# Kernel tuning notes

Hardware: AMD Instinct MI355X
Metric: run time of the kernel (lower is better)

Reference implementation:

```python
import jax, jax.numpy as jnp
import numpy as np

D = 128          # embedding_size
K = 1024         # num_embedding
DECAY = 0.99
EPS = 1e-5
VQ_COMMIT = 0.25
B, T = 16, 4096


def setup_inputs() -> dict:
    key = jax.random.key(0)
    k1, k2, k3 = jax.random.split(key, 3)
    emb = jax.random.normal(k2, (D, K), dtype=jnp.float32)
    return {
        "input": jax.random.normal(k1, (B, T, D), dtype=jnp.float32),
        "embedding": emb,
        "cluster_size": jnp.zeros((K,), dtype=jnp.float32),
        "embedding_mean": emb.copy(),
    }


def reference(input, embedding, cluster_size, embedding_mean):
    # ---- quantize: squared-distance argmin over codebook ----
    flatten = input.reshape(-1, D)                                   # [N, D]
    dist = ((flatten ** 2).sum(1, keepdims=True)
            - 2.0 * flatten @ embedding
            + (embedding ** 2).sum(0, keepdims=True))                # [N, K]
    embedding_ind = jnp.argmin(dist, axis=1)                         # [N]
    code = embedding_ind.reshape(input.shape[:-1])                   # [B, T]

    # ---- dequantize: codebook gather ----
    quantize = jnp.take(embedding.T, code, axis=0)                   # [B, T, D]

    # ---- EMA codebook update (training mode) ----
    N = flatten.shape[0]
    counts = jax.ops.segment_sum(jnp.ones((N,), input.dtype), embedding_ind,
                                 num_segments=K)                     # [K]
    emb_sum = jax.ops.segment_sum(flatten, embedding_ind,
                                  num_segments=K).T                  # [D, K]
    new_cluster_size = cluster_size * DECAY + (1.0 - DECAY) * counts
    new_embedding_mean = embedding_mean * DECAY + (1.0 - DECAY) * emb_sum
    n = new_cluster_size.sum()
    cs = (new_cluster_size + EPS) / (n + K * EPS) * n
    new_embedding = new_embedding_mean / cs[None, :]                 # [D, K]

    # ---- straight-through estimator + commitment loss ----
    quantize_st = input + jax.lax.stop_gradient(quantize - input)
    diff = VQ_COMMIT * jnp.mean(
        (jax.lax.stop_gradient(quantize_st) - input) ** 2)

    return (quantize_st, diff, code,
            new_embedding, new_cluster_size, new_embedding_mean)
```

## Files before the change

### kernel.cpp

```cpp
#include <hip/hip_runtime.h>
#include <hip/hip_fp16.h>
#include <math.h>

#define D_ 128
#define K_ 1024
#define N_ 65536
#define DECAY_ 0.99f
#define OMD_ 0.01f
#define EPS_ 1e-5f
#define VQC_ 0.25f
#define M1_ 0.14f
#define M2_ 0.14f
#define BIAS_ 96.0f
#define CLMIN_ 0.5f
#define CLMAX_ 508.0f
#define WSEG 32

typedef __attribute__((ext_vector_type(8))) _Float16 half8;
typedef __attribute__((ext_vector_type(4))) float f32x4;

#define WOFF_CODE  0
#define WOFF_E2    65536
#define WOFF_CNT   66560
#define WOFF_SSQ   67584
#define WOFF_RCNT  67585
#define WOFF_BASE  67648
#define WOFF_CURS  68736
#define WOFF_ORDER 69760
#define WOFF_ET    136320
#define WOFF_PART  267392
#define WOFF_CSORT 398464
#define WOFF_RLIST 791680
#define WOFF_EF    857216

#define OOFF_Q     0
#define OOFF_DIFF  8388608
#define OOFF_CODE  8388609
#define OOFF_NEMB  8454145
#define OOFF_NCS   8585217
#define OOFF_NMEAN 8586241

__device__ __forceinline__ unsigned umin32(unsigned a, unsigned b) { return a < b ? a : b; }
__device__ __forceinline__ unsigned umax32(unsigned a, unsigned b) { return a > b ? a : b; }

__device__ __forceinline__ void gld16(const unsigned short* g, unsigned short* l) {
    __builtin_amdgcn_global_load_lds(
        (const __attribute__((address_space(1))) unsigned int*)g,
        (__attribute__((address_space(3))) unsigned int*)l, 16, 0, 0);
}

__launch_bounds__(256)
__global__ void k_prep(const float* __restrict__ E, float* __restrict__ Et,
                       unsigned short* __restrict__ Ef, float* __restrict__ e2,
                       int* __restrict__ cnt, float* __restrict__ part1) {
    __shared__ float tile[128 * 17];
    __shared__ float e2s[16];
    int tid = threadIdx.x;
    int b = blockIdx.x;
    int c0 = b * 16;
    if (b == 0) {
        for (int i = tid; i < 1026; i += 256) cnt[i] = 0;
    }
    #pragma unroll
    for (int i = 0; i < 8; ++i) part1[b * 2048 + i * 256 + tid] = 0.f;
    if (tid < 16) e2s[tid] = 0.f;
    #pragma unroll
    for (int i = 0; i < 8; ++i) {
        int idx = i * 256 + tid;
        int d = idx >> 4, cc = idx & 15;
        tile[d * 17 + cc] = E[d * K_ + c0 + cc];
    }
    __syncthreads();
    #pragma unroll
    for (int i = 0; i < 8; ++i) {
        int idx = i * 256 + tid;
        int cc = idx >> 7, d = idx & 127;
        Et[(size_t)(c0 + cc) * D_ + d] = tile[d * 17 + cc];
    }
    int L = tid & 63, s = tid >> 6;
    int cc = L & 15;
    int d0 = s * 32 + ((L >> 4) << 3);
    unsigned short h[8];
    float sq = 0.f;
    #pragma unroll
    for (int j = 0; j < 8; ++j) {
        float e = tile[(d0 + j) * 17 + cc];
        sq = fmaf(e, e, sq);
        h[j] = __half_as_ushort(__float2half(-2.f * e));
    }
    int T = b * 256 + tid;
    #pragma unroll
    for (int j = 0; j < 8; ++j) Ef[T * 8 + j] = h[j];
    atomicAdd(&e2s[cc], sq);
    __syncthreads();
    if (tid < 16) {
        e2[c0 + tid] = e2s[tid];
    }
}

__launch_bounds__(512, 2)
__global__ void k_argmin_mfma(const float* __restrict__ x, const unsigned short* __restrict__ Ef,
                              const float* __restrict__ e2,
                              int* __restrict__ code_i, float* __restrict__ code_f,
                              int* __restrict__ cnt, int* __restrict__ rcnt,
                              int* __restrict__ rlist, const float* __restrict__ Et) {
    __shared__ unsigned short Bs[3][8192];
    __shared__ float e2s[K_];
    int tid = threadIdx.x;
    int w = tid >> 6, L = tid & 63, quad = L >> 4, col = L & 15;
    int mg = w >> 1, ng = w & 1;
    int n0 = blockIdx.x * 128;

    for (int i = tid; i < K_; i += 512) e2s[i] = e2[i];

    half8 ah[2][4];
    #pragma unroll
    for (int mt = 0; mt < 2; ++mt) {
        int tok = n0 + (2 * mg + mt) * 16 + col;
        #pragma unroll
        for (int s = 0; s < 4; ++s) {
            const float* p = x + (size_t)tok * D_ + s * 32 + quad * 8;
            float4 u0 = *(const float4*)(p);
            float4 u1 = *(const float4*)(p + 4);
            ah[mt][s][0] = (_Float16)u0.x; ah[mt][s][1] = (_Float16)u0.y;
            ah[mt][s][2] = (_Float16)u0.z; ah[mt][s][3] = (_Float16)u0.w;
            ah[mt][s][4] = (_Float16)u1.x; ah[mt][s][5] = (_Float16)u1.y;
            ah[mt][s][6] = (_Float16)u1.z; ah[mt][s][7] = (_Float16)u1.w;
        }
    }

    unsigned k1[2][4], k2[2][4], k3[2][4];
    #pragma unroll
    for (int mt = 0; mt < 2; ++mt)
        #pragma unroll
        for (int r = 0; r < 4; ++r) {
            k1[mt][r] = 0xFFFFFFFFu; k2[mt][r] = 0xFFFFFFFFu; k3[mt][r] = 0xFFFFFFFFu;
        }

    __syncthreads();

    #pragma unroll
    for (int i = 0; i < 2; ++i) {
        int o = (w * 2 + i) * 512;
        gld16(Ef + o + L * 8, &Bs[0][o]);
    }
    #pragma unroll
    for (int i = 0; i < 2; ++i) {
        int o = (w * 2 + i) * 512;
        gld16(Ef + 8192 + o + L * 8, &Bs[1][o]);
    }

    #pragma unroll
    for (int q = 0; q < 16; ++q) {
        if (q < 15) asm volatile("s_waitcnt vmcnt(2)" ::: "memory");
        else        asm volatile("s_waitcnt vmcnt(0)" ::: "memory");
        __builtin_amdgcn_s_barrier();
        asm volatile("" ::: "memory");

        const unsigned short* Bp = &Bs[q % 3][0];

        float evb[2];
        #pragma unroll
        for (int nn = 0; nn < 2; ++nn)
            evb[nn] = e2s[q * 64 + (2 * ng + nn) * 16 + col] + BIAS_;
        f32x4 acc[2][2];
        #pragma unroll
        for (int mt = 0; mt < 2; ++mt)
            #pragma unroll
            for (int nn = 0; nn < 2; ++nn)
                #pragma unroll
                for (int r = 0; r < 4; ++r)
                    acc[mt][nn][r] = evb[nn];

        #pragma unroll
        for (int s = 0; s < 4; ++s) {
            half8 bh[2];
            #pragma unroll
            for (int nn = 0; nn < 2; ++nn) {
                int off = (((2 * ng + nn) * 4 + s) * 64 + L) * 8;
                bh[nn] = *(const half8*)(Bp + off);
            }
            #pragma unroll
            for (int nn = 0; nn < 2; ++nn)
                #pragma unroll
                for (int mt = 0; mt < 2; ++mt)
                    acc[mt][nn] = __builtin_amdgcn_mfma_f32_16x16x32_f16(ah[mt][s], bh[nn], acc[mt][nn], 0, 0, 0);
        }

        #pragma unroll
        for (int nn = 0; nn < 2; ++nn) {
            unsigned cb = (unsigned)(q * 64 + (2 * ng + nn) * 16 + col);
            #pragma unroll
            for (int mt = 0; mt < 2; ++mt)
                #pragma unroll
                for (int r = 0; r < 4; ++r) {
                    float dc = fminf(fmaxf(acc[mt][nn][r], CLMIN_), CLMAX_);
                    unsigned key = (__float_as_uint(dc) & 0xFFFFFC00u) | cb;
                    unsigned m1 = umax32(k1[mt][r], key);
                    k1[mt][r]   = umin32(k1[mt][r], key);
                    unsigned m2 = umax32(k2[mt][r], m1);
                    k2[mt][r]   = umin32(k2[mt][r], m1);
                    k3[mt][r]   = umin32(k3[mt][r], m2);
                }
        }

        if (q < 14) {
            const unsigned short* src = Ef + (q + 2) * 8192;
            int sl = (q + 2) % 3;
            #pragma unroll
            for (int i = 0; i < 2; ++i) {
                int o = (w * 2 + i) * 512;
                gld16(src + o + L * 8, &Bs[sl][o]);
            }
        }
    }

    __syncthreads();
    unsigned* mk1 = (unsigned*)&Bs[0][0];
    unsigned* mk2 = mk1 + 256;
    unsigned* mk3 = mk2 + 256;

    #pragma unroll
    for (int mt = 0; mt < 2; ++mt) {
        #pragma unroll
        for (int r = 0; r < 4; ++r) {
            unsigned a = k1[mt][r], b = k2[mt][r], c = k3[mt][r];
            #pragma unroll
            for (int m = 1; m < 16; m <<= 1) {
                unsigned ao = (unsigned)__shfl_xor((int)a, m);
                unsigned bo = (unsigned)__shfl_xor((int)b, m);
                unsigned co = (unsigned)__shfl_xor((int)c, m);
                unsigned t1 = umax32(a, ao);
                a           = umin32(a, ao);
                unsigned s2 = umin32(b, bo);
                unsigned u  = umax32(t1, s2);
                b           = umin32(t1, s2);
                c           = umin32(u, umin32(c, co));
            }
            if (col == 0) {
                int tl = (2 * mg + mt) * 16 + quad * 4 + r;
                mk1[tl * 2 + ng] = a;
                mk2[tl * 2 + ng] = b;
                mk3[tl * 2 + ng] = c;
            }
        }
    }
    __syncthreads();
    if (tid < 128) {
        unsigned a1 = mk1[tid * 2], b1 = mk1[tid * 2 + 1];
        unsigned a2 = mk2[tid * 2], b2 = mk2[tid * 2 + 1];
        unsigned a3 = mk3[tid * 2], b3 = mk3[tid * 2 + 1];
        unsigned t1 = umax32(a1, b1);
        unsigned kk1 = umin32(a1, b1);
        unsigned s2 = umin32(a2, b2);
        unsigned kk2 = umin32(t1, s2);
        unsigned u  = umax32(t1, s2);
        unsigned kk3 = umin32(u, umin32(a3, b3));

        int i1 = (int)(kk1 & 1023u), i2 = (int)(kk2 & 1023u);
        float d1 = __uint_as_float(kk1 & 0xFFFFFC00u);
        float d2 = __uint_as_float(kk2 & 0xFFFFFC00u);
        float d3 = __uint_as_float(kk3 & 0xFFFFFC00u);
        int tok = n0 + tid;

        if (d3 - d1 < M2_) {
            code_i[tok] = i1;
            code_f[tok] = (float)i1;
            atomicAdd(cnt + i1, 1);
            int p = atomicAdd(rcnt, 1);
            rlist[p] = tok;
        } else {
            int win = i1;
            if (d2 - d1 < M1_) {
                const float* xr = x  + (size_t)tok * D_;
                const float* ea = Et + (size_t)i1 * D_;
                const float* eb = Et + (size_t)i2 * D_;
                float s1 = 0.f, sB = 0.f;
                #pragma unroll 4
                for (int dd = 0; dd < D_; dd += 4) {
                    float4 xv = *(const float4*)(xr + dd);
                    float4 av = *(const float4*)(ea + dd);
                    float4 bv = *(const float4*)(eb + dd);
                    s1 = fmaf(xv.x, av.x, s1); s1 = fmaf(xv.y, av.y, s1);
                    s1 = fmaf(xv.z, av.z, s1); s1 = fmaf(xv.w, av.w, s1);
                    sB = fmaf(xv.x, bv.x, sB); sB = fmaf(xv.y, bv.y, sB);
                    sB = fmaf(xv.z, bv.z, sB); sB = fmaf(xv.w, bv.w, sB);
                }
                float ex1 = e2s[i1] - 2.f * s1;
                float ex2 = e2s[i2] - 2.f * sB;
                if (ex2 < ex1 || (ex2 == ex1 && i2 < i1)) win = i2;
            }
            code_i[tok] = win;
            code_f[tok] = (float)win;
            atomicAdd(cnt + win, 1);
        }
    }
}

__launch_bounds__(256)
__global__ void k_fix(const float* __restrict__ x, const float* __restrict__ Et,
                      const float* __restrict__ e2, const int* __restrict__ rcnt,
                      const int* __restrict__ rlist, int* __restrict__ code_i,
                      float* __restrict__ code_f, int* __restrict__ cnt) {
    __shared__ float4 xs[32];
    __shared__ float sd[8];
    __shared__ int   si[8];
    int tid = threadIdx.x;
    int lane = tid & 63, w = tid >> 6;
    int half = lane >> 5;
    int q32  = lane & 31;
    int slot = w * 2 + half;
    int nr = *rcnt;
    for (int it = blockIdx.x; it < nr; it += gridDim.x) {
        __syncthreads();
        int tok = rlist[it];
        if (tid < 32) xs[tid] = ((const float4*)(x + (size_t)tok * D_))[tid];
        __syncthreads();
        float4 xv = xs[q32];
        float bd = INFINITY; int bb = 0;
        for (int c0 = 0; c0 < K_; c0 += 8) {
            int c = c0 + slot;
            float4 e = ((const float4*)(Et + (size_t)c * D_))[q32];
            float dot = xv.x * e.x + xv.y * e.y + xv.z * e.z + xv.w * e.w;
            dot += __shfl_xor(dot, 1);
            dot += __shfl_xor(dot, 2);
            dot += __shfl_xor(dot, 4);
            dot += __shfl_xor(dot, 8);
            dot += __shfl_xor(dot, 16);
            float dist = e2[c] - 2.f * dot;
            if (dist < bd) { bd = dist; bb = c; }
        }
        if (q32 == 0) { sd[slot] = bd; si[slot] = bb; }
        __syncthreads();
        if (tid == 0) {
            float fb = sd[0]; int fi = si[0];
            #pragma unroll
            for (int s = 1; s < 8; ++s) {
                if (sd[s] < fb || (sd[s] == fb && si[s] < fi)) { fb = sd[s]; fi = si[s]; }
            }
            int ob = code_i[tok];
            if (fi != ob) {
                code_i[tok] = fi;
                code_f[tok] = (float)fi;
                atomicAdd(cnt + ob, -1);
                atomicAdd(cnt + fi, 1);
            }
        }
    }
}

__launch_bounds__(256)
__global__ void k_scan(const int* __restrict__ cnt, int* __restrict__ base,
                       int* __restrict__ cursor) {
    int t = threadIdx.x;
    int lane = t & 63, wv = t >> 6;
    int c[4];
    #pragma unroll
    for (int j = 0; j < 4; ++j) c[j] = cnt[4 * t + j];
    int s = c[0] + c[1] + c[2] + c[3];
    int ps = s;
    #pragma unroll
    for (int m = 1; m < 64; m <<= 1) {
        int o = __shfl_up(ps, m);
        if (lane >= m) ps += o;
    }
    __shared__ int wtot[4];
    if (lane == 63) wtot[wv] = ps;
    __syncthreads();
    int woff = 0;
    for (int i = 0; i < 4; ++i) if (i < wv) woff += wtot[i];
    int run = woff + ps - s;
    #pragma unroll
    for (int j = 0; j < 4; ++j) {
        cursor[4 * t + j] = run;
        run += c[j];
        base[4 * t + j + 1] = run;
    }
    if (t == 0) base[0] = 0;
}

__global__ void k_scatter(const int* __restrict__ code_i, int* __restrict__ cursor,
                          int* __restrict__ order, int* __restrict__ csort) {
    int n = blockIdx.x * 256 + threadIdx.x;
    int c = code_i[n];
    int pos = atomicAdd(cursor + c, 1);
    order[pos] = n;
    csort[pos] = c;
}

__launch_bounds__(128)
__global__ void k_segdeq(const float* __restrict__ x, const float* __restrict__ Et,
                         const int* __restrict__ order, const int* __restrict__ csort,
                         float* __restrict__ part1, float* __restrict__ outq,
                         float* __restrict__ ssqp) {
    __shared__ int sn[WSEG], sc[WSEG];
    int d = threadIdx.x;
    int i0 = blockIdx.x * WSEG;
    if (d < WSEG) { sn[d] = order[i0 + d]; sc[d] = csort[i0 + d]; }
    __syncthreads();
    int cprev = sc[0];
    float eq = Et[(size_t)cprev * D_ + d];
    float acc = 0.f, ssql = 0.f;
    float xv = x[(size_t)sn[0] * D_ + d];
    #pragma unroll 4
    for (int j = 0; j < WSEG; ++j) {
        float xn = (j < WSEG - 1) ? x[(size_t)sn[j + 1] * D_ + d] : 0.f;
        int c = sc[j];
        if (c != cprev) {
            atomicAdd(&part1[(size_t)cprev * D_ + d], acc);
            acc = 0.f;
            eq = Et[(size_t)c * D_ + d];
            cprev = c;
        }
        float qv = xv + (eq - xv);
        outq[(size_t)sn[j] * D_ + d] = qv;
        float t = qv - xv;
        ssql = fmaf(t, t, ssql);
        acc += xv;
        xv = xn;
    }
    atomicAdd(&part1[(size_t)cprev * D_ + d], acc);

    #pragma unroll
    for (int off = 32; off > 0; off >>= 1) ssql += __shfl_down(ssql, off);
    __shared__ float wsum[2];
    if ((d & 63) == 0) wsum[d >> 6] = ssql;
    __syncthreads();
    if (d == 0) atomicAdd(ssqp, wsum[0] + wsum[1]);
}

__launch_bounds__(256)
__global__ void k_embed(const float* __restrict__ em, const float* __restrict__ part1,
                        const int* __restrict__ cnt, const float* __restrict__ csz,
                        const float* __restrict__ ssqp, float* __restrict__ out_nmean,
                        float* __restrict__ out_nemb, float* __restrict__ out_ncs,
                        float* __restrict__ out_diff) {
    int tid = threadIdx.x;
    __shared__ float red[256];

    float ls = 0.f;
    for (int j = tid; j < K_; j += 256) ls += csz[j] * DECAY_ + OMD_ * (float)cnt[j];
    red[tid] = ls;
    __syncthreads();
    for (int off = 128; off > 0; off >>= 1) {
        if (tid < off) red[tid] += red[tid + off];
        __syncthreads();
    }
    float n = red[0];
    __syncthreads();

    if (blockIdx.x == 0) {
        for (int j = tid; j < K_; j += 256)
            out_ncs[j] = csz[j] * DECAY_ + OMD_ * (float)cnt[j];
        if (tid == 0) *out_diff = VQC_ * ssqp[0] / (float)(N_ * D_);
    }

    int i = blockIdx.x * 256 + tid;
    int k = i & (K_ - 1);
    int d = i >> 10;
    float ncs_k = csz[k] * DECAY_ + OMD_ * (float)cnt[k];
    float csk = (ncs_k + EPS_) / (n + (float)K_ * EPS_) * n;
    float es = part1[(size_t)k * D_ + d];
    float nm = em[i] * DECAY_ + OMD_ * es;
    out_nmean[i] = nm;
    out_nemb[i]  = nm / csk;
}

extern "C" void kernel_launch(void* const* d_in, const int* in_sizes, int n_in,
                              void* d_out, int out_size, void* d_ws, size_t ws_size,
                              hipStream_t stream) {
    const float* x   = (const float*)d_in[0];
    const float* E   = (const float*)d_in[1];
    const float* csz = (const float*)d_in[2];
    const float* em  = (const float*)d_in[3];
    float* out = (float*)d_out;
    float* W   = (float*)d_ws;

    int*   code_i = (int*)(W + WOFF_CODE);
    float* e2     = W + WOFF_E2;
    int*   cnt    = (int*)(W + WOFF_CNT);
    float* ssqp   = W + WOFF_SSQ;
    int*   rcnt   = (int*)(W + WOFF_RCNT);
    int*   base   = (int*)(W + WOFF_BASE);
    int*   cursor = (int*)(W + WOFF_CURS);
    int*   order  = (int*)(W + WOFF_ORDER);
    float* Et     = W + WOFF_ET;
    float* part1  = W + WOFF_PART;
    int*   csort  = (int*)(W + WOFF_CSORT);
    int*   rlist  = (int*)(W + WOFF_RLIST);
    unsigned short* Ef = (unsigned short*)(W + WOFF_EF);

    k_prep<<<64, 256, 0, stream>>>(E, Et, Ef, e2, cnt, part1);
    k_argmin_mfma<<<N_ / 128, 512, 0, stream>>>(x, Ef, e2, code_i,
                                                out + OOFF_CODE, cnt, rcnt, rlist, Et);
    k_fix<<<1024, 256, 0, stream>>>(x, Et, e2, rcnt, rlist, code_i, out + OOFF_CODE, cnt);
    k_scan<<<1, 256, 0, stream>>>(cnt, base, cursor);
    k_scatter<<<N_ / 256, 256, 0, stream>>>(code_i, cursor, order, csort);
    k_segdeq<<<N_ / WSEG, 128, 0, stream>>>(x, Et, order, csort, part1,
                                            out + OOFF_Q, ssqp);
    k_embed<<<(D_ * K_) / 256, 256, 0, stream>>>(em, part1, cnt, csz, ssqp,
                                                 out + OOFF_NMEAN, out + OOFF_NEMB,
                                                 out + OOFF_NCS, out + OOFF_DIFF);
}
```

Before: 238.8 us.

## Fuse scan, scatter, segment dequant and EMA update into one cooperative kernel

Replaces four kernel launches (scan, scatter, segmented dequantize/sum, EMA update) with one cooperative kernel of 2048 blocks that uses grid.sync between phases. Each block recomputes the prefix scan into shared memory, so the single-block scan kernel goes away. A separate zeroed counter array replaces the cursor array. Separately, the argmin kernel's launch bound is raised to ask for 4 blocks per CU. This trades launch gaps for grid-wide barriers and needs all 2048 blocks co-resident, and the tighter occupancy target may force register spills in the MFMA argmin.

```diff
diff --git a/kernel.cpp b/kernel.cpp
--- a/kernel.cpp
+++ b/kernel.cpp
@@ -1,6 +1,9 @@
 #include <hip/hip_runtime.h>
 #include <hip/hip_fp16.h>
+#include <hip/hip_cooperative_groups.h>
 #include <math.h>
+
+namespace cg = cooperative_groups;
 
 #define D_ 128
 #define K_ 1024
@@ -15,6 +18,7 @@
 #define CLMIN_ 0.5f
 #define CLMAX_ 508.0f
 #define WSEG 32
+#define CBLK 2048
 
 typedef __attribute__((ext_vector_type(8))) _Float16 half8;
 typedef __attribute__((ext_vector_type(4))) float f32x4;
@@ -52,7 +56,8 @@
 __launch_bounds__(256)
 __global__ void k_prep(const float* __restrict__ E, float* __restrict__ Et,
                        unsigned short* __restrict__ Ef, float* __restrict__ e2,
-                       int* __restrict__ cnt, float* __restrict__ part1) {
+                       int* __restrict__ cnt, int* __restrict__ zc,
+                       float* __restrict__ part1) {
     __shared__ float tile[128 * 17];
     __shared__ float e2s[16];
     int tid = threadIdx.x;
@@ -61,6 +66,9 @@
     if (b == 0) {
         for (int i = tid; i < 1026; i += 256) cnt[i] = 0;
     }
+    if (b == 1) {
+        for (int i = tid; i < 1024; i += 256) zc[i] = 0;
+    }
     #pragma unroll
     for (int i = 0; i < 8; ++i) part1[b * 2048 + i * 256 + tid] = 0.f;
     if (tid < 16) e2s[tid] = 0.f;
@@ -98,7 +106,7 @@
     }
 }
 
-__launch_bounds__(512, 2)
+__launch_bounds__(512, 4)
 __global__ void k_argmin_mfma(const float* __restrict__ x, const unsigned short* __restrict__ Ef,
                               const float* __restrict__ e2,
                               int* __restrict__ code_i, float* __restrict__ code_f,
@@ -349,121 +357,123 @@
     }
 }
 
-__launch_bounds__(256)
-__global__ void k_scan(const int* __restrict__ cnt, int* __restrict__ base,
-                       int* __restrict__ cursor) {
-    int t = threadIdx.x;
-    int lane = t & 63, wv = t >> 6;
-    int c[4];
-    #pragma unroll
-    for (int j = 0; j < 4; ++j) c[j] = cnt[4 * t + j];
-    int s = c[0] + c[1] + c[2] + c[3];
+__launch_bounds__(128)
+__global__ void k_coop(const int* __restrict__ cnt, int* __restrict__ zc,
+                       const int* __restrict__ code_i, int* __restrict__ order,
+                       int* __restrict__ csort, const float* __restrict__ x,
+                       const float* __restrict__ Et, float* __restrict__ part1,
+                       float* __restrict__ outq, float* __restrict__ ssqp,
+                       const float* __restrict__ em, const float* __restrict__ csz,
+                       float* __restrict__ out_nmean, float* __restrict__ out_nemb,
+                       float* __restrict__ out_ncs, float* __restrict__ out_diff) {
+    cg::grid_group grid = cg::this_grid();
+    __shared__ int baseS[1025];
+    __shared__ int sn[WSEG], sc[WSEG];
+    __shared__ float red[128];
+    int tid = threadIdx.x;
+    int bid = blockIdx.x;
+    int lane = tid & 63, wv = tid >> 6;
+
+    int c8[8];
+    #pragma unroll
+    for (int j = 0; j < 8; ++j) c8[j] = cnt[8 * tid + j];
+    int s = 0;
+    #pragma unroll
+    for (int j = 0; j < 8; ++j) s += c8[j];
     int ps = s;
     #pragma unroll
     for (int m = 1; m < 64; m <<= 1) {
         int o = __shfl_up(ps, m);
         if (lane >= m) ps += o;
     }
-    __shared__ int wtot[4];
+    __shared__ int wtot[2];
     if (lane == 63) wtot[wv] = ps;
     __syncthreads();
-    int woff = 0;
-    for (int i = 0; i < 4; ++i) if (i < wv) woff += wtot[i];
+    int woff = (wv == 1) ? wtot[0] : 0;
     int run = woff + ps - s;
     #pragma unroll
-    for (int j = 0; j < 4; ++j) {
-        cursor[4 * t + j] = run;
-        run += c[j];
-        base[4 * t + j + 1] = run;
-    }
-    if (t == 0) base[0] = 0;
-}
-
-__global__ void k_scatter(const int* __restrict__ code_i, int* __restrict__ cursor,
-                          int* __restrict__ order, int* __restrict__ csort) {
-    int n = blockIdx.x * 256 + threadIdx.x;
-    int c = code_i[n];
-    int pos = atomicAdd(cursor + c, 1);
-    order[pos] = n;
-    csort[pos] = c;
-}
-
-__launch_bounds__(128)
-__global__ void k_segdeq(const float* __restrict__ x, const float* __restrict__ Et,
-                         const int* __restrict__ order, const int* __restrict__ csort,
-                         float* __restrict__ part1, float* __restrict__ outq,
-                         float* __restrict__ ssqp) {
-    __shared__ int sn[WSEG], sc[WSEG];
-    int d = threadIdx.x;
-    int i0 = blockIdx.x * WSEG;
-    if (d < WSEG) { sn[d] = order[i0 + d]; sc[d] = csort[i0 + d]; }
-    __syncthreads();
-    int cprev = sc[0];
-    float eq = Et[(size_t)cprev * D_ + d];
-    float acc = 0.f, ssql = 0.f;
-    float xv = x[(size_t)sn[0] * D_ + d];
-    #pragma unroll 4
-    for (int j = 0; j < WSEG; ++j) {
-        float xn = (j < WSEG - 1) ? x[(size_t)sn[j + 1] * D_ + d] : 0.f;
-        int c = sc[j];
-        if (c != cprev) {
-            atomicAdd(&part1[(size_t)cprev * D_ + d], acc);
-            acc = 0.f;
-            eq = Et[(size_t)c * D_ + d];
-            cprev = c;
-        }
-        float qv = xv + (eq - xv);
-        outq[(size_t)sn[j] * D_ + d] = qv;
-        float t = qv - xv;
-        ssql = fmaf(t, t, ssql);
-        acc += xv;
-        xv = xn;
-    }
-    atomicAdd(&part1[(size_t)cprev * D_ + d], acc);
-
-    #pragma unroll
-    for (int off = 32; off > 0; off >>= 1) ssql += __shfl_down(ssql, off);
-    __shared__ float wsum[2];
-    if ((d & 63) == 0) wsum[d >> 6] = ssql;
-    __syncthreads();
-    if (d == 0) atomicAdd(ssqp, wsum[0] + wsum[1]);
-}
-
-__launch_bounds__(256)
-__global__ void k_embed(const float* __restrict__ em, const float* __restrict__ part1,
-                        const int* __restrict__ cnt, const float* __restrict__ csz,
-                        const float* __restrict__ ssqp, float* __restrict__ out_nmean,
-                        float* __restrict__ out_nemb, float* __restrict__ out_ncs,
-                        float* __restrict__ out_diff) {
-    int tid = threadIdx.x;
-    __shared__ float red[256];
-
-    float ls = 0.f;
-    for (int j = tid; j < K_; j += 256) ls += csz[j] * DECAY_ + OMD_ * (float)cnt[j];
-    red[tid] = ls;
-    __syncthreads();
-    for (int off = 128; off > 0; off >>= 1) {
-        if (tid < off) red[tid] += red[tid + off];
+    for (int j = 0; j < 8; ++j) {
+        run += c8[j];
+        baseS[8 * tid + j + 1] = run;
+    }
+    if (tid == 0) baseS[0] = 0;
+    __syncthreads();
+
+    if (bid < 512) {
+        int n = bid * 128 + tid;
+        int c = code_i[n];
+        int pos = baseS[c] + atomicAdd(zc + c, 1);
+        order[pos] = n;
+        csort[pos] = c;
+    }
+    grid.sync();
+
+    {
+        int d = tid;
+        int i0 = bid * WSEG;
+        if (d < WSEG) { sn[d] = order[i0 + d]; sc[d] = csort[i0 + d]; }
         __syncthreads();
-    }
-    float n = red[0];
-    __syncthreads();
-
-    if (blockIdx.x == 0) {
-        for (int j = tid; j < K_; j += 256)
-            out_ncs[j] = csz[j] * DECAY_ + OMD_ * (float)cnt[j];
-        if (tid == 0) *out_diff = VQC_ * ssqp[0] / (float)(N_ * D_);
-    }
-
-    int i = blockIdx.x * 256 + tid;
-    int k = i & (K_ - 1);
-    int d = i >> 10;
-    float ncs_k = csz[k] * DECAY_ + OMD_ * (float)cnt[k];
-    float csk = (ncs_k + EPS_) / (n + (float)K_ * EPS_) * n;
-    float es = part1[(size_t)k * D_ + d];
-    float nm = em[i] * DECAY_ + OMD_ * es;
-    out_nmean[i] = nm;
-    out_nemb[i]  = nm / csk;
+        int cprev = sc[0];
+        float eq = Et[(size_t)cprev * D_ + d];
+        float acc = 0.f, ssql = 0.f;
+        float xv = x[(size_t)sn[0] * D_ + d];
+        #pragma unroll 4
+        for (int j = 0; j < WSEG; ++j) {
+            float xn = (j < WSEG - 1) ? x[(size_t)sn[j + 1] * D_ + d] : 0.f;
+            int c = sc[j];
+            if (c != cprev) {
+                atomicAdd(&part1[(size_t)cprev * D_ + d], acc);
+                acc = 0.f;
+                eq = Et[(size_t)c * D_ + d];
+                cprev = c;
+            }
+            float qv = xv + (eq - xv);
+            outq[(size_t)sn[j] * D_ + d] = qv;
+            float t = qv - xv;
+            ssql = fmaf(t, t, ssql);
+            acc += xv;
+            xv = xn;
+        }
+        atomicAdd(&part1[(size_t)cprev * D_ + d], acc);
+
+        #pragma unroll
+        for (int off = 32; off > 0; off >>= 1) ssql += __shfl_down(ssql, off);
+        __shared__ float wsum[2];
+        if ((d & 63) == 0) wsum[d >> 6] = ssql;
+        __syncthreads();
+        if (d == 0) atomicAdd(ssqp, wsum[0] + wsum[1]);
+    }
+    grid.sync();
+
+    {
+        float ls = 0.f;
+        for (int j = tid; j < K_; j += 128) ls += csz[j] * DECAY_ + OMD_ * (float)cnt[j];
+        red[tid] = ls;
+        __syncthreads();
+        for (int off = 64; off > 0; off >>= 1) {
+            if (tid < off) red[tid] += red[tid + off];
+            __syncthreads();
+        }
+        float n = red[0];
+
+        if (bid == 0) {
+            for (int j = tid; j < K_; j += 128)
+                out_ncs[j] = csz[j] * DECAY_ + OMD_ * (float)cnt[j];
+            if (tid == 0) *out_diff = VQC_ * ssqp[0] / (float)(N_ * D_);
+        }
+
+        if (bid < 1024) {
+            int i = bid * 128 + tid;
+            int k = i & (K_ - 1);
+            int d = i >> 10;
+            float ncs_k = csz[k] * DECAY_ + OMD_ * (float)cnt[k];
+            float csk = (ncs_k + EPS_) / (n + (float)K_ * EPS_) * n;
+            float es = part1[(size_t)k * D_ + d];
+            float nm = em[i] * DECAY_ + OMD_ * es;
+            out_nmean[i] = nm;
+            out_nemb[i]  = nm / csk;
+        }
+    }
 }
 
 extern "C" void kernel_launch(void* const* d_in, const int* in_sizes, int n_in,
@@ -481,8 +491,7 @@
     int*   cnt    = (int*)(W + WOFF_CNT);
     float* ssqp   = W + WOFF_SSQ;
     int*   rcnt   = (int*)(W + WOFF_RCNT);
-    int*   base   = (int*)(W + WOFF_BASE);
-    int*   cursor = (int*)(W + WOFF_CURS);
+    int*   zc     = (int*)(W + WOFF_CURS);
     int*   order  = (int*)(W + WOFF_ORDER);
     float* Et     = W + WOFF_ET;
     float* part1  = W + WOFF_PART;
@@ -490,15 +499,19 @@
     int*   rlist  = (int*)(W + WOFF_RLIST);
     unsigned short* Ef = (unsigned short*)(W + WOFF_EF);
 
-    k_prep<<<64, 256, 0, stream>>>(E, Et, Ef, e2, cnt, part1);
-    k_argmin_mfma<<<N_ / 128, 512, 0, stream>>>(x, Ef, e2, code_i,
-                                                out + OOFF_CODE, cnt, rcnt, rlist, Et);
-    k_fix<<<1024, 256, 0, stream>>>(x, Et, e2, rcnt, rlist, code_i, out + OOFF_CODE, cnt);
-    k_scan<<<1, 256, 0, stream>>>(cnt, base, cursor);
-    k_scatter<<<N_ / 256, 256, 0, stream>>>(code_i, cursor, order, csort);
-    k_segdeq<<<N_ / WSEG, 128, 0, stream>>>(x, Et, order, csort, part1,
-                                            out + OOFF_Q, ssqp);
-    k_embed<<<(D_ * K_) / 256, 256, 0, stream>>>(em, part1, cnt, csz, ssqp,
-                                                 out + OOFF_NMEAN, out + OOFF_NEMB,
-                                                 out + OOFF_NCS, out + OOFF_DIFF);
+    float* code_o = out + OOFF_CODE;
+    float* outq   = out + OOFF_Q;
+    float* nmean  = out + OOFF_NMEAN;
+    float* nemb   = out + OOFF_NEMB;
+    float* ncs    = out + OOFF_NCS;
+    float* diffp  = out + OOFF_DIFF;
+
+    k_prep<<<64, 256, 0, stream>>>(E, Et, Ef, e2, cnt, zc, part1);
+    k_argmin_mfma<<<N_ / 128, 512, 0, stream>>>(x, Ef, e2, code_i, code_o,
+                                                cnt, rcnt, rlist, Et);
+    k_fix<<<1024, 256, 0, stream>>>(x, Et, e2, rcnt, rlist, code_i, code_o, cnt);
+
+    void* args[] = { &cnt, &zc, &code_i, &order, &csort, &x, &Et, &part1,
+                     &outq, &ssqp, &em, &csz, &nmean, &nemb, &ncs, &diffp };
+    hipLaunchCooperativeKernel((void*)k_coop, dim3(CBLK), dim3(128), args, 0, stream);
 }
```

Measured after the change: 556.6 us. 133% more time.

## Load codebook fragments directly from global memory, drop LDS pipeline in argmin

Applied to the files above, without the earlier changes.

The argmin kernel no longer stages codebook tiles into a triple-buffered LDS ring with async global-to-LDS loads and barriers. Each wave now reads its B fragments straight from global memory (L2/L1 cached) and covers all 64 codes per step for its own 32 tokens. The cross-wave top-3 merge goes away because each token is owned by one wave. The block shrinks from 512 to 256 threads. This removes LDS traffic and per-step barriers, but every wave now fetches the whole codebook itself, so global/L2 load traffic rises and load latency is exposed, with only 2x unrolling to hide it.

```diff
diff --git a/kernel.cpp b/kernel.cpp
--- a/kernel.cpp
+++ b/kernel.cpp
@@ -43,12 +43,6 @@
 __device__ __forceinline__ unsigned umin32(unsigned a, unsigned b) { return a < b ? a : b; }
 __device__ __forceinline__ unsigned umax32(unsigned a, unsigned b) { return a > b ? a : b; }
 
-__device__ __forceinline__ void gld16(const unsigned short* g, unsigned short* l) {
-    __builtin_amdgcn_global_load_lds(
-        (const __attribute__((address_space(1))) unsigned int*)g,
-        (__attribute__((address_space(3))) unsigned int*)l, 16, 0, 0);
-}
-
 __launch_bounds__(256)
 __global__ void k_prep(const float* __restrict__ E, float* __restrict__ Et,
                        unsigned short* __restrict__ Ef, float* __restrict__ e2,
@@ -98,25 +92,24 @@
     }
 }
 
-__launch_bounds__(512, 2)
+__launch_bounds__(256)
 __global__ void k_argmin_mfma(const float* __restrict__ x, const unsigned short* __restrict__ Ef,
                               const float* __restrict__ e2,
                               int* __restrict__ code_i, float* __restrict__ code_f,
                               int* __restrict__ cnt, int* __restrict__ rcnt,
                               int* __restrict__ rlist, const float* __restrict__ Et) {
-    __shared__ unsigned short Bs[3][8192];
     __shared__ float e2s[K_];
+    __shared__ unsigned mk1[128], mk2[128], mk3[128];
     int tid = threadIdx.x;
     int w = tid >> 6, L = tid & 63, quad = L >> 4, col = L & 15;
-    int mg = w >> 1, ng = w & 1;
-    int n0 = blockIdx.x * 128;
-
-    for (int i = tid; i < K_; i += 512) e2s[i] = e2[i];
+    int n0 = blockIdx.x * 128 + w * 32;
+
+    for (int i = tid; i < K_; i += 256) e2s[i] = e2[i];
 
     half8 ah[2][4];
     #pragma unroll
     for (int mt = 0; mt < 2; ++mt) {
-        int tok = n0 + (2 * mg + mt) * 16 + col;
+        int tok = n0 + mt * 16 + col;
         #pragma unroll
         for (int s = 0; s < 4; ++s) {
             const float* p = x + (size_t)tok * D_ + s * 32 + quad * 8;
@@ -139,62 +132,39 @@
 
     __syncthreads();
 
-    #pragma unroll
-    for (int i = 0; i < 2; ++i) {
-        int o = (w * 2 + i) * 512;
-        gld16(Ef + o + L * 8, &Bs[0][o]);
-    }
-    #pragma unroll
-    for (int i = 0; i < 2; ++i) {
-        int o = (w * 2 + i) * 512;
-        gld16(Ef + 8192 + o + L * 8, &Bs[1][o]);
-    }
-
-    #pragma unroll
+    #pragma unroll 2
     for (int q = 0; q < 16; ++q) {
-        if (q < 15) asm volatile("s_waitcnt vmcnt(2)" ::: "memory");
-        else        asm volatile("s_waitcnt vmcnt(0)" ::: "memory");
-        __builtin_amdgcn_s_barrier();
-        asm volatile("" ::: "memory");
-
-        const unsigned short* Bp = &Bs[q % 3][0];
-
-        float evb[2];
-        #pragma unroll
-        for (int nn = 0; nn < 2; ++nn)
-            evb[nn] = e2s[q * 64 + (2 * ng + nn) * 16 + col] + BIAS_;
-        f32x4 acc[2][2];
-        #pragma unroll
-        for (int mt = 0; mt < 2; ++mt)
+        const unsigned short* Bq = Ef + (size_t)q * 8192;
+
+        f32x4 acc[2][4];
+        #pragma unroll
+        for (int g = 0; g < 4; ++g) {
+            float ev = e2s[q * 64 + g * 16 + col] + BIAS_;
+            acc[0][g] = (f32x4){ev, ev, ev, ev};
+            acc[1][g] = (f32x4){ev, ev, ev, ev};
+        }
+
+        #pragma unroll
+        for (int s = 0; s < 4; ++s) {
+            half8 bh[4];
             #pragma unroll
-            for (int nn = 0; nn < 2; ++nn)
-                #pragma unroll
-                for (int r = 0; r < 4; ++r)
-                    acc[mt][nn][r] = evb[nn];
-
-        #pragma unroll
-        for (int s = 0; s < 4; ++s) {
-            half8 bh[2];
+            for (int g = 0; g < 4; ++g)
+                bh[g] = *(const half8*)(Bq + ((g * 4 + s) * 64 + L) * 8);
             #pragma unroll
-            for (int nn = 0; nn < 2; ++nn) {
-                int off = (((2 * ng + nn) * 4 + s) * 64 + L) * 8;
-                bh[nn] = *(const half8*)(Bp + off);
-            }
-            #pragma unroll
-            for (int nn = 0; nn < 2; ++nn)
-                #pragma unroll
-                for (int mt = 0; mt < 2; ++mt)
-                    acc[mt][nn] = __builtin_amdgcn_mfma_f32_16x16x32_f16(ah[mt][s], bh[nn], acc[mt][nn], 0, 0, 0);
-        }
-
-        #pragma unroll
-        for (int nn = 0; nn < 2; ++nn) {
-            unsigned cb = (unsigned)(q * 64 + (2 * ng + nn) * 16 + col);
+            for (int g = 0; g < 4; ++g) {
+                acc[0][g] = __builtin_amdgcn_mfma_f32_16x16x32_f16(ah[0][s], bh[g], acc[0][g], 0, 0, 0);
+                acc[1][g] = __builtin_amdgcn_mfma_f32_16x16x32_f16(ah[1][s], bh[g], acc[1][g], 0, 0, 0);
+            }
+        }
+
+        #pragma unroll
+        for (int g = 0; g < 4; ++g) {
+            unsigned cb = (unsigned)(q * 64 + g * 16 + col);
             #pragma unroll
             for (int mt = 0; mt < 2; ++mt)
                 #pragma unroll
                 for (int r = 0; r < 4; ++r) {
-                    float dc = fminf(fmaxf(acc[mt][nn][r], CLMIN_), CLMAX_);
+                    float dc = fminf(fmaxf(acc[mt][g][r], CLMIN_), CLMAX_);
                     unsigned key = (__float_as_uint(dc) & 0xFFFFFC00u) | cb;
                     unsigned m1 = umax32(k1[mt][r], key);
                     k1[mt][r]   = umin32(k1[mt][r], key);
@@ -203,22 +173,7 @@
                     k3[mt][r]   = umin32(k3[mt][r], m2);
                 }
         }
-
-        if (q < 14) {
-            const unsigned short* src = Ef + (q + 2) * 8192;
-            int sl = (q + 2) % 3;
-            #pragma unroll
-            for (int i = 0; i < 2; ++i) {
-                int o = (w * 2 + i) * 512;
-                gld16(src + o + L * 8, &Bs[sl][o]);
-            }
-        }
-    }
-
-    __syncthreads();
-    unsigned* mk1 = (unsigned*)&Bs[0][0];
-    unsigned* mk2 = mk1 + 256;
-    unsigned* mk3 = mk2 + 256;
+    }
 
     #pragma unroll
     for (int mt = 0; mt < 2; ++mt) {
@@ -238,30 +193,21 @@
                 c           = umin32(u, umin32(c, co));
             }
             if (col == 0) {
-                int tl = (2 * mg + mt) * 16 + quad * 4 + r;
-                mk1[tl * 2 + ng] = a;
-                mk2[tl * 2 + ng] = b;
-                mk3[tl * 2 + ng] = c;
+                int tl = w * 32 + mt * 16 + quad * 4 + r;
+                mk1[tl] = a;
+                mk2[tl] = b;
+                mk3[tl] = c;
             }
         }
     }
     __syncthreads();
     if (tid < 128) {
-        unsigned a1 = mk1[tid * 2], b1 = mk1[tid * 2 + 1];
-        unsigned a2 = mk2[tid * 2], b2 = mk2[tid * 2 + 1];
-        unsigned a3 = mk3[tid * 2], b3 = mk3[tid * 2 + 1];
-        unsigned t1 = umax32(a1, b1);
-        unsigned kk1 = umin32(a1, b1);
-        unsigned s2 = umin32(a2, b2);
-        unsigned kk2 = umin32(t1, s2);
-        unsigned u  = umax32(t1, s2);
-        unsigned kk3 = umin32(u, umin32(a3, b3));
-
+        unsigned kk1 = mk1[tid], kk2 = mk2[tid], kk3 = mk3[tid];
         int i1 = (int)(kk1 & 1023u), i2 = (int)(kk2 & 1023u);
         float d1 = __uint_as_float(kk1 & 0xFFFFFC00u);
         float d2 = __uint_as_float(kk2 & 0xFFFFFC00u);
         float d3 = __uint_as_float(kk3 & 0xFFFFFC00u);
-        int tok = n0 + tid;
+        int tok = blockIdx.x * 128 + tid;
 
         if (d3 - d1 < M2_) {
             code_i[tok] = i1;
@@ -491,7 +437,7 @@
     unsigned short* Ef = (unsigned short*)(W + WOFF_EF);
 
     k_prep<<<64, 256, 0, stream>>>(E, Et, Ef, e2, cnt, part1);
-    k_argmin_mfma<<<N_ / 128, 512, 0, stream>>>(x, Ef, e2, code_i,
+    k_argmin_mfma<<<N_ / 128, 256, 0, stream>>>(x, Ef, e2, code_i,
                                                 out + OOFF_CODE, cnt, rcnt, rlist, Et);
     k_fix<<<1024, 256, 0, stream>>>(x, Et, e2, rcnt, rlist, code_i, out + OOFF_CODE, cnt);
     k_scan<<<1, 256, 0, stream>>>(cnt, base, cursor);
```

Measured after the change: 248.7 us. 1.04x slower.
